# Performance work log

Measured on AMD Instinct MI355X. Metric: run time of the kernel, lower is better.

## Reference

```python
import jax, jax.numpy as jnp
from jax import lax
import numpy as np

THRESH = 0.5
R = 4  # suppression radius -> (2R+1)^3 max-pool window


def setup_inputs() -> dict:
    key = jax.random.key(0)
    pred_vol = jax.random.uniform(key, (1, 1, 64, 512, 512), dtype=jnp.float32)
    return {"pred_vol": pred_vol}


def reference(pred_vol):
    # Threshold: keep values above thresh, zero otherwise
    pred_thresh = jnp.where(pred_vol > THRESH, pred_vol, jnp.float32(0.0))
    # 3D max-pool, kernel 2R+1, stride 1, padding R (pad with -inf so padding
    k = 2 * R + 1
    conf = lax.reduce_window(
        pred_thresh,
        -jnp.inf,
        lax.max,
        window_dimensions=(1, 1, k, k, k),
        window_strides=(1, 1, 1, 1, 1),
        padding=[(0, 0), (0, 0), (R, R), (R, R), (R, R)],
    )
    # Keep only strict local maxima of the thresholded volume
    conf = jnp.where((conf > 0.0) & (conf == pred_thresh), conf, jnp.float32(0.0))
    return jnp.squeeze(conf)  # [D, H, W]
```

## Files before the change

### kernel.cpp

```cpp
#include <hip/hip_runtime.h>

static constexpr int Dd = 64;
static constexpr int Hh = 512;
static constexpr int Ww = 512;
static constexpr int RAD = 4;
static constexpr float THRESH_V = 0.5f;
static constexpr int W4 = Ww / 4;
static constexpr int PLANE4 = Hh * W4;

static constexpr int TH = 4;
static constexpr int DC = 16;
static constexpr int ROWS = TH + 2 * RAD;
static constexpr int NPL = DC + 2 * RAD;
static constexpr int NBLK = (Hh / TH) * (Dd / DC);

typedef float nf4 __attribute__((ext_vector_type(4)));

__device__ __forceinline__ float4 f4max(float4 a, float4 b) {
    return make_float4(fmaxf(a.x, b.x), fmaxf(a.y, b.y), fmaxf(a.z, b.z), fmaxf(a.w, b.w));
}
__device__ __forceinline__ int iclamp(int v, int lo, int hi) {
    return v < lo ? lo : (v > hi ? hi : v);
}

#define BAR_VM(N) asm volatile("s_waitcnt vmcnt(" #N ") lgkmcnt(0)\n\ts_barrier" ::: "memory")
#define BAR_LDS() asm volatile("s_waitcnt lgkmcnt(0)\n\ts_barrier" ::: "memory")

__device__ __forceinline__ void load_lds16(const float4* g, float4* l) {
    __builtin_amdgcn_global_load_lds(
        (const __attribute__((address_space(1))) void*)g,
        (__attribute__((address_space(3))) void*)l, 16, 0, 0);
}

__global__ __launch_bounds__(512, 2)
void fused_nms_k5(const float4* __restrict__ x4, float4* __restrict__ o4) {
    __shared__ float4 braw[3][ROWS * W4];
    __shared__ float4 bcol[TH * W4];

    const int tid  = threadIdx.x;
    const int w4   = tid & (W4 - 1);
    const int hr   = tid >> 7;
    const int wid  = tid >> 6;
    const int lane = tid & 63;

    const int b    = blockIdx.x;
    const int band = b & 7;
    const int rest = b >> 3;
    const int ht   = band * 16 + (rest & 15);
    const int dc   = rest >> 4;
    const int h0   = ht * TH;
    const int d0   = dc * DC;

    const int colm = w4 ? w4 - 1 : 0;
    const int colp = (w4 < W4 - 1) ? w4 + 1 : W4 - 1;
    const int outrow = (h0 + hr) * W4 + w4;

    int goff[3], loff[3];
#pragma unroll
    for (int k = 0; k < 3; ++k) {
        const int s    = wid + 8 * k;
        const int row  = s >> 1;
        const int half = s & 1;
        const int gh   = iclamp(h0 - RAD + row, 0, Hh - 1);
        goff[k] = gh * W4 + half * 64 + lane;
        loff[k] = row * W4 + half * 64;
    }

    auto stage = [&](int p) {
        const int gd = iclamp(d0 - RAD + p, 0, Dd - 1);
        const float4* pl = x4 + (size_t)gd * PLANE4;
        float4* dst = braw[p % 3];
#pragma unroll
        for (int k = 0; k < 3; ++k)
            load_lds16(pl + goff[k], dst + loff[k]);
    };

    float4 R[8];
    float4 C[4];

    stage(0);
    stage(1);

#pragma unroll
    for (int t = 0; t < NPL; ++t) {
        const bool doE = (t >= 8);

        if (t <= 8)       { BAR_VM(3); }
        else if (t == 9)  { BAR_VM(4); }
        else if (t <= 22) { BAR_VM(5); }
        else              { BAR_VM(2); }

        if (t + 2 < NPL) stage(t + 2);
        __builtin_amdgcn_sched_barrier(0);

        const float4* Bc = &braw[t % 3][hr * W4 + w4];
        float4 q0 = Bc[0 * W4], q1 = Bc[1 * W4], q2 = Bc[2 * W4], q3 = Bc[3 * W4];
        float4 c4 = Bc[4 * W4];
        float4 q5 = Bc[5 * W4], q6 = Bc[6 * W4], q7 = Bc[7 * W4], q8 = Bc[8 * W4];
        float4 m = f4max(f4max(f4max(q0, q1), f4max(q2, q3)),
                         f4max(f4max(c4, q5), f4max(f4max(q6, q7), q8)));
        bcol[hr * W4 + w4] = m;
        BAR_LDS();

        const float4 lm = bcol[hr * W4 + colm];
        const float4 rm = bcol[hr * W4 + colp];
        const float l3 = lm.w, l2 = fmaxf(lm.z, l3), l1 = fmaxf(lm.y, l2), l0 = fmaxf(lm.x, l1);
        const float core = fmaxf(fmaxf(m.x, m.y), fmaxf(m.z, m.w));
        const float r0 = rm.x, r1 = fmaxf(r0, rm.y), r2 = fmaxf(r1, rm.z), r3 = fmaxf(r2, rm.w);
        float4 pm;
        pm.x = fmaxf(l0, fmaxf(core, r0));
        pm.y = fmaxf(l1, fmaxf(core, r1));
        pm.z = fmaxf(l2, fmaxf(core, r2));
        pm.w = fmaxf(l3, fmaxf(core, r3));

        if (doE) {
            const float4 cen = C[t & 3];
            float4 mm = pm;
#pragma unroll
            for (int i = 0; i < 8; ++i) mm = f4max(mm, R[i]);
            nf4 q;
            q.x = (cen.x > THRESH_V && cen.x == mm.x) ? cen.x : 0.0f;
            q.y = (cen.y > THRESH_V && cen.y == mm.y) ? cen.y : 0.0f;
            q.z = (cen.z > THRESH_V && cen.z == mm.z) ? cen.z : 0.0f;
            q.w = (cen.w > THRESH_V && cen.w == mm.w) ? cen.w : 0.0f;
            __builtin_nontemporal_store(
                q, (nf4*)&o4[(size_t)(d0 + t - 8) * PLANE4 + outrow]);
        }
        R[t & 7] = pm;
        C[t & 3] = c4;
    }
}

extern "C" void kernel_launch(void* const* d_in, const int* in_sizes, int n_in,
                              void* d_out, int out_size, void* d_ws, size_t ws_size,
                              hipStream_t stream) {
    const float4* x4 = (const float4*)d_in[0];
    float4* out4 = (float4*)d_out;
    (void)d_ws; (void)ws_size; (void)in_sizes; (void)n_in; (void)out_size;
    fused_nms_k5<<<dim3(NBLK), dim3(512), 0, stream>>>(x4, out4);
}
```

Before: 114.9 us.

## Process two output rows per thread with taller H tile to share vertical max

Doubles the H tile height to 8 rows, so each thread now computes two adjacent output rows. The two rows share the 8-row core of their vertical max, which cuts LDS reads and max operations per output. The H halo overhead of global loads also shrinks, since 16 rows are staged per plane for 8 outputs instead of 12 for 4. In exchange it doubles register use for the depth ring buffers, and with launch bounds lowered to 1 block per CU, occupancy and latency hiding may drop.

Result: slower. 118.9 us (+3.5%).

```diff
diff --git a/kernel.cpp b/kernel.cpp
--- a/kernel.cpp
+++ b/kernel.cpp
@@ -8,7 +8,7 @@
 static constexpr int W4 = Ww / 4;
 static constexpr int PLANE4 = Hh * W4;
 
-static constexpr int TH = 4;
+static constexpr int TH = 8;
 static constexpr int DC = 16;
 static constexpr int ROWS = TH + 2 * RAD;
 static constexpr int NPL = DC + 2 * RAD;
@@ -32,32 +32,31 @@
         (__attribute__((address_space(3))) void*)l, 16, 0, 0);
 }
 
-__global__ __launch_bounds__(512, 2)
-void fused_nms_k5(const float4* __restrict__ x4, float4* __restrict__ o4) {
+__global__ __launch_bounds__(512, 1)
+void fused_nms_k6(const float4* __restrict__ x4, float4* __restrict__ o4) {
     __shared__ float4 braw[3][ROWS * W4];
     __shared__ float4 bcol[TH * W4];
 
     const int tid  = threadIdx.x;
     const int w4   = tid & (W4 - 1);
-    const int hr   = tid >> 7;
+    const int hs   = tid >> 7;
     const int wid  = tid >> 6;
     const int lane = tid & 63;
 
     const int b    = blockIdx.x;
     const int band = b & 7;
     const int rest = b >> 3;
-    const int ht   = band * 16 + (rest & 15);
-    const int dc   = rest >> 4;
+    const int ht   = band * 8 + (rest & 7);
+    const int dc   = rest >> 3;
     const int h0   = ht * TH;
     const int d0   = dc * DC;
 
     const int colm = w4 ? w4 - 1 : 0;
     const int colp = (w4 < W4 - 1) ? w4 + 1 : W4 - 1;
-    const int outrow = (h0 + hr) * W4 + w4;
 
-    int goff[3], loff[3];
+    int goff[4], loff[4];
 #pragma unroll
-    for (int k = 0; k < 3; ++k) {
+    for (int k = 0; k < 4; ++k) {
         const int s    = wid + 8 * k;
         const int row  = s >> 1;
         const int half = s & 1;
@@ -71,12 +70,24 @@
         const float4* pl = x4 + (size_t)gd * PLANE4;
         float4* dst = braw[p % 3];
 #pragma unroll
-        for (int k = 0; k < 3; ++k)
+        for (int k = 0; k < 4; ++k)
             load_lds16(pl + goff[k], dst + loff[k]);
     };
 
-    float4 R[8];
-    float4 C[4];
+    auto hwin = [&](const float4 lm, const float4 cm, const float4 rm) -> float4 {
+        const float l3 = lm.w, l2 = fmaxf(lm.z, l3), l1 = fmaxf(lm.y, l2), l0 = fmaxf(lm.x, l1);
+        const float core = fmaxf(fmaxf(cm.x, cm.y), fmaxf(cm.z, cm.w));
+        const float q0 = rm.x, q1 = fmaxf(q0, rm.y), q2 = fmaxf(q1, rm.z), q3 = fmaxf(q2, rm.w);
+        float4 pm;
+        pm.x = fmaxf(l0, fmaxf(core, q0));
+        pm.y = fmaxf(l1, fmaxf(core, q1));
+        pm.z = fmaxf(l2, fmaxf(core, q2));
+        pm.w = fmaxf(l3, fmaxf(core, q3));
+        return pm;
+    };
+
+    float4 R0[8], R1[8];
+    float4 C0[4], C1[4];
 
     stage(0);
     stage(1);
@@ -85,49 +96,50 @@
     for (int t = 0; t < NPL; ++t) {
         const bool doE = (t >= 8);
 
-        if (t <= 8)       { BAR_VM(3); }
-        else if (t == 9)  { BAR_VM(4); }
-        else if (t <= 22) { BAR_VM(5); }
-        else              { BAR_VM(2); }
+        if (t <= 8)       { BAR_VM(4); }
+        else if (t == 9)  { BAR_VM(6); }
+        else if (t <= 22) { BAR_VM(8); }
+        else              { BAR_VM(4); }
 
         if (t + 2 < NPL) stage(t + 2);
         __builtin_amdgcn_sched_barrier(0);
 
-        const float4* Bc = &braw[t % 3][hr * W4 + w4];
-        float4 q0 = Bc[0 * W4], q1 = Bc[1 * W4], q2 = Bc[2 * W4], q3 = Bc[3 * W4];
-        float4 c4 = Bc[4 * W4];
-        float4 q5 = Bc[5 * W4], q6 = Bc[6 * W4], q7 = Bc[7 * W4], q8 = Bc[8 * W4];
-        float4 m = f4max(f4max(f4max(q0, q1), f4max(q2, q3)),
-                         f4max(f4max(c4, q5), f4max(f4max(q6, q7), q8)));
-        bcol[hr * W4 + w4] = m;
+        const float4* Bc = &braw[t % 3][(2 * hs) * W4 + w4];
+        float4 r0 = Bc[0 * W4], r1 = Bc[1 * W4], r2 = Bc[2 * W4], r3 = Bc[3 * W4];
+        float4 r4 = Bc[4 * W4], r5 = Bc[5 * W4], r6 = Bc[6 * W4], r7 = Bc[7 * W4];
+        float4 r8 = Bc[8 * W4], r9 = Bc[9 * W4];
+        float4 core = f4max(f4max(f4max(r1, r2), f4max(r3, r4)),
+                            f4max(f4max(r5, r6), f4max(r7, r8)));
+        float4 v0 = f4max(core, r0);
+        float4 v1 = f4max(core, r9);
+        bcol[(2 * hs) * W4 + w4]     = v0;
+        bcol[(2 * hs + 1) * W4 + w4] = v1;
         BAR_LDS();
 
-        const float4 lm = bcol[hr * W4 + colm];
-        const float4 rm = bcol[hr * W4 + colp];
-        const float l3 = lm.w, l2 = fmaxf(lm.z, l3), l1 = fmaxf(lm.y, l2), l0 = fmaxf(lm.x, l1);
-        const float core = fmaxf(fmaxf(m.x, m.y), fmaxf(m.z, m.w));
-        const float r0 = rm.x, r1 = fmaxf(r0, rm.y), r2 = fmaxf(r1, rm.z), r3 = fmaxf(r2, rm.w);
-        float4 pm;
-        pm.x = fmaxf(l0, fmaxf(core, r0));
-        pm.y = fmaxf(l1, fmaxf(core, r1));
-        pm.z = fmaxf(l2, fmaxf(core, r2));
-        pm.w = fmaxf(l3, fmaxf(core, r3));
+        const float4 pm0 = hwin(bcol[(2 * hs) * W4 + colm],     v0, bcol[(2 * hs) * W4 + colp]);
+        const float4 pm1 = hwin(bcol[(2 * hs + 1) * W4 + colm], v1, bcol[(2 * hs + 1) * W4 + colp]);
 
         if (doE) {
-            const float4 cen = C[t & 3];
-            float4 mm = pm;
+            const float4 cen0 = C0[t & 3];
+            const float4 cen1 = C1[t & 3];
+            float4 mm0 = pm0, mm1 = pm1;
 #pragma unroll
-            for (int i = 0; i < 8; ++i) mm = f4max(mm, R[i]);
-            nf4 q;
-            q.x = (cen.x > THRESH_V && cen.x == mm.x) ? cen.x : 0.0f;
-            q.y = (cen.y > THRESH_V && cen.y == mm.y) ? cen.y : 0.0f;
-            q.z = (cen.z > THRESH_V && cen.z == mm.z) ? cen.z : 0.0f;
-            q.w = (cen.w > THRESH_V && cen.w == mm.w) ? cen.w : 0.0f;
-            __builtin_nontemporal_store(
-                q, (nf4*)&o4[(size_t)(d0 + t - 8) * PLANE4 + outrow]);
+            for (int i = 0; i < 8; ++i) { mm0 = f4max(mm0, R0[i]); mm1 = f4max(mm1, R1[i]); }
+            const size_t obase = (size_t)(d0 + t - 8) * PLANE4 + (size_t)(h0 + 2 * hs) * W4 + w4;
+            nf4 q0, q1;
+            q0.x = (cen0.x > THRESH_V && cen0.x == mm0.x) ? cen0.x : 0.0f;
+            q0.y = (cen0.y > THRESH_V && cen0.y == mm0.y) ? cen0.y : 0.0f;
+            q0.z = (cen0.z > THRESH_V && cen0.z == mm0.z) ? cen0.z : 0.0f;
+            q0.w = (cen0.w > THRESH_V && cen0.w == mm0.w) ? cen0.w : 0.0f;
+            q1.x = (cen1.x > THRESH_V && cen1.x == mm1.x) ? cen1.x : 0.0f;
+            q1.y = (cen1.y > THRESH_V && cen1.y == mm1.y) ? cen1.y : 0.0f;
+            q1.z = (cen1.z > THRESH_V && cen1.z == mm1.z) ? cen1.z : 0.0f;
+            q1.w = (cen1.w > THRESH_V && cen1.w == mm1.w) ? cen1.w : 0.0f;
+            __builtin_nontemporal_store(q0, (nf4*)&o4[obase]);
+            __builtin_nontemporal_store(q1, (nf4*)&o4[obase + W4]);
         }
-        R[t & 7] = pm;
-        C[t & 3] = c4;
+        R0[t & 7] = pm0;  R1[t & 7] = pm1;
+        C0[t & 3] = r4;   C1[t & 3] = r5;
     }
 }
 
@@ -137,5 +149,5 @@
     const float4* x4 = (const float4*)d_in[0];
     float4* out4 = (float4*)d_out;
     (void)d_ws; (void)ws_size; (void)in_sizes; (void)n_in; (void)out_size;
-    fused_nms_k5<<<dim3(NBLK), dim3(512), 0, stream>>>(x4, out4);
+    fused_nms_k6<<<dim3(NBLK), dim3(512), 0, stream>>>(x4, out4);
 }
```

## Use DPP lane shifts for horizontal max and software-pipeline vertical/horizontal stages

Applied to the files above, without the earlier changes.

Replaces the per-plane LDS round-trip for neighbour column maxima with DPP wave-wide shift operations, exchanging only the two half-row boundary values through a small double-buffered LDS patch. The horizontal pass is skewed one iteration behind the vertical pass so that the barrier already present for staging also covers the patch exchange. This removes one LDS barrier and the full row write/read per plane. In exchange it adds an extra loop iteration, more live registers, and relies on wave_shr/shl DPP behaviour across the whole 64-lane wave.

Measured after the change: 124.9 us. +8.7%, slower.

```diff
diff --git a/kernel.cpp b/kernel.cpp
--- a/kernel.cpp
+++ b/kernel.cpp
@@ -23,6 +23,22 @@
     return v < lo ? lo : (v > hi ? hi : v);
 }
 
+static constexpr int DPP_WAVE_SHR1 = 0x138;
+static constexpr int DPP_WAVE_SHL1 = 0x130;
+template <int CTRL>
+__device__ __forceinline__ float4 f4dpp(float4 v) {
+    float4 r;
+    r.x = __int_as_float(__builtin_amdgcn_update_dpp(
+        __float_as_int(v.x), __float_as_int(v.x), CTRL, 0xF, 0xF, false));
+    r.y = __int_as_float(__builtin_amdgcn_update_dpp(
+        __float_as_int(v.y), __float_as_int(v.y), CTRL, 0xF, 0xF, false));
+    r.z = __int_as_float(__builtin_amdgcn_update_dpp(
+        __float_as_int(v.z), __float_as_int(v.z), CTRL, 0xF, 0xF, false));
+    r.w = __int_as_float(__builtin_amdgcn_update_dpp(
+        __float_as_int(v.w), __float_as_int(v.w), CTRL, 0xF, 0xF, false));
+    return r;
+}
+
 #define BAR_VM(N) asm volatile("s_waitcnt vmcnt(" #N ") lgkmcnt(0)\n\ts_barrier" ::: "memory")
 #define BAR_LDS() asm volatile("s_waitcnt lgkmcnt(0)\n\ts_barrier" ::: "memory")
 
@@ -33,9 +49,9 @@
 }
 
 __global__ __launch_bounds__(512, 2)
-void fused_nms_k5(const float4* __restrict__ x4, float4* __restrict__ o4) {
+void fused_nms_k9(const float4* __restrict__ x4, float4* __restrict__ o4) {
     __shared__ float4 braw[3][ROWS * W4];
-    __shared__ float4 bcol[TH * W4];
+    __shared__ float4 bpatch[2][TH][2];
 
     const int tid  = threadIdx.x;
     const int w4   = tid & (W4 - 1);
@@ -50,9 +66,6 @@
     const int dc   = rest >> 4;
     const int h0   = ht * TH;
     const int d0   = dc * DC;
-
-    const int colm = w4 ? w4 - 1 : 0;
-    const int colp = (w4 < W4 - 1) ? w4 + 1 : W4 - 1;
     const int outrow = (h0 + hr) * W4 + w4;
 
     int goff[3], loff[3];
@@ -76,58 +89,75 @@
     };
 
     float4 R[8];
-    float4 C[4];
+    float4 C[5];
+    float4 vp;
 
     stage(0);
     stage(1);
 
 #pragma unroll
-    for (int t = 0; t < NPL; ++t) {
-        const bool doE = (t >= 8);
+    for (int t = 0; t <= NPL; ++t) {
+        const bool doV = (t <= NPL - 1);
+        const bool doH = (t >= 1);
+        const bool doE = (t >= 9);
 
-        if (t <= 8)       { BAR_VM(3); }
-        else if (t == 9)  { BAR_VM(4); }
+        if (t <= 9)       { BAR_VM(3); }
+        else if (t == 10) { BAR_VM(4); }
         else if (t <= 22) { BAR_VM(5); }
-        else              { BAR_VM(2); }
+        else if (t == 23) { BAR_VM(2); }
+        else              { BAR_LDS(); }
 
-        if (t + 2 < NPL) stage(t + 2);
+        if (t + 2 <= NPL - 1) stage(t + 2);
         __builtin_amdgcn_sched_barrier(0);
 
-        const float4* Bc = &braw[t % 3][hr * W4 + w4];
-        float4 q0 = Bc[0 * W4], q1 = Bc[1 * W4], q2 = Bc[2 * W4], q3 = Bc[3 * W4];
-        float4 c4 = Bc[4 * W4];
-        float4 q5 = Bc[5 * W4], q6 = Bc[6 * W4], q7 = Bc[7 * W4], q8 = Bc[8 * W4];
-        float4 m = f4max(f4max(f4max(q0, q1), f4max(q2, q3)),
-                         f4max(f4max(c4, q5), f4max(f4max(q6, q7), q8)));
-        bcol[hr * W4 + w4] = m;
-        BAR_LDS();
+        float4 nv, nc;
+        if (doV) {
+            const float4* Bc = &braw[t % 3][tid];
+            float4 r0 = Bc[0 * W4], r1 = Bc[1 * W4], r2 = Bc[2 * W4], r3 = Bc[3 * W4];
+            float4 r4 = Bc[4 * W4];
+            float4 r5 = Bc[5 * W4], r6 = Bc[6 * W4], r7 = Bc[7 * W4], r8 = Bc[8 * W4];
+            nv = f4max(f4max(f4max(r0, r1), f4max(r2, r3)),
+                       f4max(f4max(r4, r5), f4max(f4max(r6, r7), r8)));
+            nc = r4;
+            if (w4 == 63) bpatch[t & 1][hr][0] = nv;
+            if (w4 == 64) bpatch[t & 1][hr][1] = nv;
+        }
 
-        const float4 lm = bcol[hr * W4 + colm];
-        const float4 rm = bcol[hr * W4 + colp];
-        const float l3 = lm.w, l2 = fmaxf(lm.z, l3), l1 = fmaxf(lm.y, l2), l0 = fmaxf(lm.x, l1);
-        const float core = fmaxf(fmaxf(m.x, m.y), fmaxf(m.z, m.w));
-        const float r0 = rm.x, r1 = fmaxf(r0, rm.y), r2 = fmaxf(r1, rm.z), r3 = fmaxf(r2, rm.w);
-        float4 pm;
-        pm.x = fmaxf(l0, fmaxf(core, r0));
-        pm.y = fmaxf(l1, fmaxf(core, r1));
-        pm.z = fmaxf(l2, fmaxf(core, r2));
-        pm.w = fmaxf(l3, fmaxf(core, r3));
+        if (doH) {
+            const int p1 = (t - 1) & 1;
+            float4 lm = f4dpp<DPP_WAVE_SHR1>(vp);
+            float4 rm = f4dpp<DPP_WAVE_SHL1>(vp);
+            if (w4 == 64) lm = bpatch[p1][hr][0];
+            if (w4 == 63) rm = bpatch[p1][hr][1];
+            const float l3 = lm.w, l2 = fmaxf(lm.z, l3), l1 = fmaxf(lm.y, l2), l0 = fmaxf(lm.x, l1);
+            const float core = fmaxf(fmaxf(vp.x, vp.y), fmaxf(vp.z, vp.w));
+            const float q0 = rm.x, q1 = fmaxf(q0, rm.y), q2 = fmaxf(q1, rm.z), q3 = fmaxf(q2, rm.w);
+            float4 pm;
+            pm.x = fmaxf(l0, fmaxf(core, q0));
+            pm.y = fmaxf(l1, fmaxf(core, q1));
+            pm.z = fmaxf(l2, fmaxf(core, q2));
+            pm.w = fmaxf(l3, fmaxf(core, q3));
 
-        if (doE) {
-            const float4 cen = C[t & 3];
-            float4 mm = pm;
+            if (doE) {
+                const float4 cen = C[t % 5];
+                float4 mm = pm;
 #pragma unroll
-            for (int i = 0; i < 8; ++i) mm = f4max(mm, R[i]);
-            nf4 q;
-            q.x = (cen.x > THRESH_V && cen.x == mm.x) ? cen.x : 0.0f;
-            q.y = (cen.y > THRESH_V && cen.y == mm.y) ? cen.y : 0.0f;
-            q.z = (cen.z > THRESH_V && cen.z == mm.z) ? cen.z : 0.0f;
-            q.w = (cen.w > THRESH_V && cen.w == mm.w) ? cen.w : 0.0f;
-            __builtin_nontemporal_store(
-                q, (nf4*)&o4[(size_t)(d0 + t - 8) * PLANE4 + outrow]);
+                for (int i = 0; i < 8; ++i) mm = f4max(mm, R[i]);
+                nf4 q;
+                q.x = (cen.x > THRESH_V && cen.x == mm.x) ? cen.x : 0.0f;
+                q.y = (cen.y > THRESH_V && cen.y == mm.y) ? cen.y : 0.0f;
+                q.z = (cen.z > THRESH_V && cen.z == mm.z) ? cen.z : 0.0f;
+                q.w = (cen.w > THRESH_V && cen.w == mm.w) ? cen.w : 0.0f;
+                __builtin_nontemporal_store(
+                    q, (nf4*)&o4[(size_t)(d0 + t - 9) * PLANE4 + outrow]);
+            }
+            R[(t - 1) & 7] = pm;
         }
-        R[t & 7] = pm;
-        C[t & 3] = c4;
+
+        if (doV) {
+            vp = nv;
+            C[t % 5] = nc;
+        }
     }
 }
 
@@ -137,5 +167,5 @@
     const float4* x4 = (const float4*)d_in[0];
     float4* out4 = (float4*)d_out;
     (void)d_ws; (void)ws_size; (void)in_sizes; (void)n_in; (void)out_size;
-    fused_nms_k5<<<dim3(NBLK), dim3(512), 0, stream>>>(x4, out4);
+    fused_nms_k9<<<dim3(NBLK), dim3(512), 0, stream>>>(x4, out4);
 }
```

## Do W-axis max in registers from global loads, drop second LDS barrier

Applied to the files above, without the earlier changes.

Switches from direct global-to-LDS loads to register loads that fetch the left, centre and right float4 neighbours from global memory, so the horizontal 9-wide max is computed before writing to LDS. This removes the per-plane bcol buffer and its second barrier, and uses a double-buffered LDS tile that holds W-reduced rows, reduced over H per step. The price is three times as many global loads (mostly cache hits) and a shallower prefetch of one plane ahead held in registers, which lowers load latency hiding and raises register pressure.

After: 138.5 us. +20.6%, slower.

```diff
diff --git a/kernel.cpp b/kernel.cpp
--- a/kernel.cpp
+++ b/kernel.cpp
@@ -24,24 +24,18 @@
 }
 
 #define BAR_VM(N) asm volatile("s_waitcnt vmcnt(" #N ") lgkmcnt(0)\n\ts_barrier" ::: "memory")
-#define BAR_LDS() asm volatile("s_waitcnt lgkmcnt(0)\n\ts_barrier" ::: "memory")
-
-__device__ __forceinline__ void load_lds16(const float4* g, float4* l) {
-    __builtin_amdgcn_global_load_lds(
-        (const __attribute__((address_space(1))) void*)g,
-        (__attribute__((address_space(3))) void*)l, 16, 0, 0);
-}
 
 __global__ __launch_bounds__(512, 2)
-void fused_nms_k5(const float4* __restrict__ x4, float4* __restrict__ o4) {
-    __shared__ float4 braw[3][ROWS * W4];
-    __shared__ float4 bcol[TH * W4];
+void fused_nms_k11(const float4* __restrict__ x4, float4* __restrict__ o4) {
+    __shared__ float4 wm[2][ROWS * W4];
 
     const int tid  = threadIdx.x;
     const int w4   = tid & (W4 - 1);
     const int hr   = tid >> 7;
     const int wid  = tid >> 6;
     const int lane = tid & 63;
+    const int q    = wid >> 1;
+    const int hh   = wid & 1;
 
     const int b    = blockIdx.x;
     const int band = b & 7;
@@ -50,84 +44,90 @@
     const int dc   = rest >> 4;
     const int h0   = ht * TH;
     const int d0   = dc * DC;
-
-    const int colm = w4 ? w4 - 1 : 0;
-    const int colp = (w4 < W4 - 1) ? w4 + 1 : W4 - 1;
     const int outrow = (h0 + hr) * W4 + w4;
 
-    int goff[3], loff[3];
+    int gl[3], gm[3], gr[3], lw[3];
+    const int rowk0 = q, rowk1 = 4 + q, rowk2 = 8 + q;
+    const int rks[3] = {rowk0, rowk1, rowk2};
 #pragma unroll
     for (int k = 0; k < 3; ++k) {
-        const int s    = wid + 8 * k;
-        const int row  = s >> 1;
-        const int half = s & 1;
-        const int gh   = iclamp(h0 - RAD + row, 0, Hh - 1);
-        goff[k] = gh * W4 + half * 64 + lane;
-        loff[k] = row * W4 + half * 64;
+        const int gh = iclamp(h0 - RAD + rks[k], 0, Hh - 1);
+        const int c  = hh * 64 + lane;
+        gm[k] = gh * W4 + c;
+        gl[k] = gh * W4 + (c ? c - 1 : 0);
+        gr[k] = gh * W4 + (c < W4 - 1 ? c + 1 : W4 - 1);
+        lw[k] = rks[k] * W4 + c;
     }
 
-    auto stage = [&](int p) {
-        const int gd = iclamp(d0 - RAD + p, 0, Dd - 1);
-        const float4* pl = x4 + (size_t)gd * PLANE4;
-        float4* dst = braw[p % 3];
+    float4 La[3], Lm[3], Lr[3];
+    auto issue = [&](int p) {
+        const float4* pl = x4 + (size_t)iclamp(d0 - RAD + p, 0, Dd - 1) * PLANE4;
 #pragma unroll
-        for (int k = 0; k < 3; ++k)
-            load_lds16(pl + goff[k], dst + loff[k]);
+        for (int k = 0; k < 3; ++k) {
+            La[k] = pl[gl[k]];
+            Lm[k] = pl[gm[k]];
+            Lr[k] = pl[gr[k]];
+        }
+    };
+    auto wmax4 = [&](float4 lm, float4 cm, float4 rm) -> float4 {
+        const float l3 = lm.w, l2 = fmaxf(lm.z, l3), l1 = fmaxf(lm.y, l2), l0 = fmaxf(lm.x, l1);
+        const float core = fmaxf(fmaxf(cm.x, cm.y), fmaxf(cm.z, cm.w));
+        const float r0 = rm.x, r1 = fmaxf(r0, rm.y), r2 = fmaxf(r1, rm.z), r3 = fmaxf(r2, rm.w);
+        float4 o;
+        o.x = fmaxf(l0, fmaxf(core, r0));
+        o.y = fmaxf(l1, fmaxf(core, r1));
+        o.z = fmaxf(l2, fmaxf(core, r2));
+        o.w = fmaxf(l3, fmaxf(core, r3));
+        return o;
     };
 
-    float4 R[8];
-    float4 C[4];
+    float4 R[8], C[6];
 
-    stage(0);
-    stage(1);
+    issue(0);
+    {
+#pragma unroll
+        for (int k = 0; k < 3; ++k) wm[0][lw[k]] = wmax4(La[k], Lm[k], Lr[k]);
+        C[0] = Lm[1];
+    }
+    issue(1);
 
 #pragma unroll
     for (int t = 0; t < NPL; ++t) {
         const bool doE = (t >= 8);
 
-        if (t <= 8)       { BAR_VM(3); }
-        else if (t == 9)  { BAR_VM(4); }
-        else if (t <= 22) { BAR_VM(5); }
-        else              { BAR_VM(2); }
+        if (t <= 8) { BAR_VM(0); } else { BAR_VM(1); }
 
-        if (t + 2 < NPL) stage(t + 2);
+        if (t + 1 < NPL) {
+            float4* dst = wm[(t + 1) & 1];
+#pragma unroll
+            for (int k = 0; k < 3; ++k) dst[lw[k]] = wmax4(La[k], Lm[k], Lr[k]);
+            C[(t + 1) % 6] = Lm[1];
+        }
+        __builtin_amdgcn_sched_barrier(0);
+        if (t + 2 < NPL) issue(t + 2);
         __builtin_amdgcn_sched_barrier(0);
 
-        const float4* Bc = &braw[t % 3][hr * W4 + w4];
-        float4 q0 = Bc[0 * W4], q1 = Bc[1 * W4], q2 = Bc[2 * W4], q3 = Bc[3 * W4];
-        float4 c4 = Bc[4 * W4];
-        float4 q5 = Bc[5 * W4], q6 = Bc[6 * W4], q7 = Bc[7 * W4], q8 = Bc[8 * W4];
-        float4 m = f4max(f4max(f4max(q0, q1), f4max(q2, q3)),
-                         f4max(f4max(c4, q5), f4max(f4max(q6, q7), q8)));
-        bcol[hr * W4 + w4] = m;
-        BAR_LDS();
-
-        const float4 lm = bcol[hr * W4 + colm];
-        const float4 rm = bcol[hr * W4 + colp];
-        const float l3 = lm.w, l2 = fmaxf(lm.z, l3), l1 = fmaxf(lm.y, l2), l0 = fmaxf(lm.x, l1);
-        const float core = fmaxf(fmaxf(m.x, m.y), fmaxf(m.z, m.w));
-        const float r0 = rm.x, r1 = fmaxf(r0, rm.y), r2 = fmaxf(r1, rm.z), r3 = fmaxf(r2, rm.w);
-        float4 pm;
-        pm.x = fmaxf(l0, fmaxf(core, r0));
-        pm.y = fmaxf(l1, fmaxf(core, r1));
-        pm.z = fmaxf(l2, fmaxf(core, r2));
-        pm.w = fmaxf(l3, fmaxf(core, r3));
+        const float4* Bc = &wm[t & 1][tid];
+        float4 r0 = Bc[0 * W4], r1 = Bc[1 * W4], r2 = Bc[2 * W4], r3 = Bc[3 * W4];
+        float4 r4 = Bc[4 * W4], r5 = Bc[5 * W4], r6 = Bc[6 * W4], r7 = Bc[7 * W4];
+        float4 r8 = Bc[8 * W4];
+        float4 pm = f4max(f4max(f4max(r0, r1), f4max(r2, r3)),
+                          f4max(f4max(r4, r5), f4max(f4max(r6, r7), r8)));
 
         if (doE) {
-            const float4 cen = C[t & 3];
+            const float4 cen = C[(t - 4) % 6];
             float4 mm = pm;
 #pragma unroll
             for (int i = 0; i < 8; ++i) mm = f4max(mm, R[i]);
-            nf4 q;
-            q.x = (cen.x > THRESH_V && cen.x == mm.x) ? cen.x : 0.0f;
-            q.y = (cen.y > THRESH_V && cen.y == mm.y) ? cen.y : 0.0f;
-            q.z = (cen.z > THRESH_V && cen.z == mm.z) ? cen.z : 0.0f;
-            q.w = (cen.w > THRESH_V && cen.w == mm.w) ? cen.w : 0.0f;
+            nf4 qv;
+            qv.x = (cen.x > THRESH_V && cen.x == mm.x) ? cen.x : 0.0f;
+            qv.y = (cen.y > THRESH_V && cen.y == mm.y) ? cen.y : 0.0f;
+            qv.z = (cen.z > THRESH_V && cen.z == mm.z) ? cen.z : 0.0f;
+            qv.w = (cen.w > THRESH_V && cen.w == mm.w) ? cen.w : 0.0f;
             __builtin_nontemporal_store(
-                q, (nf4*)&o4[(size_t)(d0 + t - 8) * PLANE4 + outrow]);
+                qv, (nf4*)&o4[(size_t)(d0 + t - 8) * PLANE4 + outrow]);
         }
         R[t & 7] = pm;
-        C[t & 3] = c4;
     }
 }
 
@@ -137,5 +137,5 @@
     const float4* x4 = (const float4*)d_in[0];
     float4* out4 = (float4*)d_out;
     (void)d_ws; (void)ws_size; (void)in_sizes; (void)n_in; (void)out_size;
-    fused_nms_k5<<<dim3(NBLK), dim3(512), 0, stream>>>(x4, out4);
+    fused_nms_k11<<<dim3(NBLK), dim3(512), 0, stream>>>(x4, out4);
 }
```
